# Optimization experiments

Measured on AMD Instinct MI355X. Metric: run time of the kernel, lower is better.

## Reference

```python
import jax, jax.numpy as jnp
import numpy as np


def setup_inputs() -> dict:
    key = jax.random.key(0)
    k1, k2, k3, k4 = jax.random.split(key, 4)
    B, Q, K, H, D = 2, 2048, 2048, 16, 128
    qs = jax.random.normal(k1, (B, Q, H, D), dtype=jnp.float32)
    ks = jax.random.normal(k2, (B, K, H, D), dtype=jnp.float32)
    vs = jax.random.normal(k3, (B, K, H, D), dtype=jnp.float32)
    valid_lens = jax.random.randint(k4, (B,), 1, K + 1, dtype=jnp.int32)
    return {"qs": qs, "ks": ks, "vs": vs, "valid_lens": valid_lens}


def reference(qs, ks, vs, valid_lens):
    B, Q, H, D = qs.shape
    K = ks.shape[1]
    # rearrange 'B L H D -> (B H) L D'
    q = qs.transpose(0, 2, 1, 3).reshape(B * H, Q, D)
    k = ks.transpose(0, 2, 1, 3).reshape(B * H, K, D)
    v = vs.transpose(0, 2, 1, 3).reshape(B * H, K, D)
    # DotScorer: scaled dot product -> (B*H, Q, K)
    scores = jnp.einsum('bqd,bkd->bqk', q, k) / jnp.sqrt(jnp.float32(D))
    # mask_attn: key positions >= valid_len get large negative score
    vl = jnp.repeat(valid_lens, H)                         # (B*H,)
    mask = jnp.arange(K)[None, None, :] < vl[:, None, None]
    scores = jnp.where(mask, scores, jnp.float32(-1e6))
    attn = jax.nn.softmax(scores, axis=-1)
    # dropout is identity (p_dropout=0 / not training)
    ctx = attn @ v                                         # (B*H, Q, D)
    ctx = ctx.reshape(B, H, Q, D).transpose(0, 2, 1, 3)    # (B, Q, H, D)
    return ctx, attn.reshape(B, H, Q, K)
```

## Files before the change

### kernel.cpp

```cpp
#include <hip/hip_runtime.h>
#include <hip/hip_bf16.h>
#include <stdint.h>

#define B_ 2
#define Qn 2048
#define Kn 2048
#define Hn 16
#define Dn 128
#define QT 128
#define KT 64
#define KT1 128
#define HD (Hn*Dn)
#define KROW 132
#define VROW 72

typedef __bf16 bf16x8 __attribute__((ext_vector_type(8)));
typedef __bf16 bf16x4 __attribute__((ext_vector_type(4)));
typedef float f32x4 __attribute__((ext_vector_type(4)));
typedef float f32x16 __attribute__((ext_vector_type(16)));

union BF8 { __bf16 e[8]; bf16x8 v; };

#define SCALE 0.088388347648318447f

struct SMp2 { unsigned short K[2][KT][KROW]; unsigned short V[2][Dn][VROW]; };
union SMu { SMp2 p2; unsigned short K1[2][KT1][KROW]; };

__device__ __forceinline__ void bar_lgkm() {
  asm volatile("s_waitcnt lgkmcnt(0)" ::: "memory");
  __builtin_amdgcn_s_barrier();
  __builtin_amdgcn_sched_barrier(0);
}

__device__ __forceinline__ bf16x4 cvt4(f32x4 a) {
  bf16x4 r;
  r[0] = (__bf16)a[0]; r[1] = (__bf16)a[1];
  r[2] = (__bf16)a[2]; r[3] = (__bf16)a[3];
  return r;
}

__device__ __forceinline__ void stage_k64(const float* kb, unsigned short (*dst)[KROW], int tid) {
  #pragma unroll
  for (int ii = 0; ii < 8; ++ii) {
    int chunk = ii * 256 + tid;
    int row = chunk >> 5, cv = chunk & 31;
    f32x4 a = *(const f32x4*)(kb + (size_t)row * HD + cv * 4);
    *(bf16x4*)&dst[row][cv * 4] = cvt4(a);
  }
}

__device__ __forceinline__ void stage_k128(const float* kb, unsigned short (*dst)[KROW], int tid) {
  #pragma unroll
  for (int ii = 0; ii < 16; ++ii) {
    int chunk = ii * 256 + tid;
    int row = chunk >> 5, cv = chunk & 31;
    f32x4 a = *(const f32x4*)(kb + (size_t)row * HD + cv * 4);
    *(bf16x4*)&dst[row][cv * 4] = cvt4(a);
  }
}

__device__ __forceinline__ void stage_v64(const float* vb, unsigned short (*dst)[VROW], int tid) {
  int d = tid & 127, t0 = tid >> 7;
  const float* colp = vb + d;
  #pragma unroll
  for (int rr = 0; rr < 4; ++rr) {
    int idx = rr * 2 + t0;
    int base = (idx >> 2) * 32 + ((idx >> 1) & 1) * 16 + (idx & 1) * 4;
    BF8 t;
    #pragma unroll
    for (int j = 0; j < 4; ++j) {
      t.e[j]     = (__bf16)colp[(size_t)(base + j) * HD];
      t.e[4 + j] = (__bf16)colp[(size_t)(base + 8 + j) * HD];
    }
    *(bf16x8*)&dst[d][idx * 8] = t.v;
  }
}

__global__ __launch_bounds__(256, 2) void attn_fwd(
    const float* __restrict__ qs, const float* __restrict__ ks,
    const float* __restrict__ vs, const int* __restrict__ vlen,
    float* __restrict__ ctx_out, float* __restrict__ attn_out)
{
  __shared__ __align__(16) SMu sm;

  const int tid = threadIdx.x, wave = tid >> 6, lane = tid & 63;
  const int l31 = lane & 31, hi = lane >> 5;

  const int L   = blockIdx.x;
  const int xcd = L & 7;
  const int i5  = L >> 3;
  const int bh  = ((i5 & 3) << 3) + xcd;
  const int qt  = i5 >> 2;
  const int b   = bh >> 4, h = bh & 15;
  const int vl  = vlen[b];
  const int qbw = qt * QT + wave * 32;

  BF8 qf[8];
  {
    const float* qrow = qs + (((size_t)(b * Qn + qbw + l31)) * Hn + h) * Dn;
    #pragma unroll
    for (int s = 0; s < 8; ++s) {
      int d0 = s * 16 + hi * 8;
      f32x4 a0 = *(const f32x4*)(qrow + d0);
      f32x4 a1 = *(const f32x4*)(qrow + d0 + 4);
      #pragma unroll
      for (int j = 0; j < 4; ++j) { qf[s].e[j] = (__bf16)a0[j]; qf[s].e[4 + j] = (__bf16)a1[j]; }
    }
  }

  const float* kbase = ks + ((size_t)b * Kn * Hn + h) * Dn;
  const float* vbase = vs + ((size_t)b * Kn * Hn + h) * Dn;

  f32x4 rsv = {0.f, 0.f, 0.f, 0.f};
  {
    const int nkt1 = (vl + KT1 - 1) / KT1;
    const bool hasb1 = (vl & (KT1 - 1)) != 0;
    stage_k128(kbase, sm.K1[0], tid);
    bar_lgkm();
    for (int t = 0; t < nkt1; ++t) {
      const int cur = t & 1;
      if (t + 1 < nkt1) stage_k128(kbase + (size_t)(t + 1) * KT1 * HD, sm.K1[cur ^ 1], tid);
      const bool mb = hasb1 && (t == nkt1 - 1);
      #pragma unroll
      for (int m = 0; m < 4; ++m) {
        f32x16 acc;
        #pragma unroll
        for (int i = 0; i < 16; ++i) acc[i] = 0.f;
        #pragma unroll
        for (int s = 0; s < 8; ++s) {
          BF8 kf; kf.v = *(const bf16x8*)&sm.K1[cur][m * 32 + l31][s * 16 + hi * 8];
          acc = __builtin_amdgcn_mfma_f32_32x32x16_bf16(kf.v, qf[s].v, acc, 0, 0, 0);
        }
        if (!mb) {
          #pragma unroll
          for (int reg = 0; reg < 16; ++reg) rsv[reg & 3] += __expf(acc[reg] * SCALE);
        } else {
          const int kb0 = t * KT1 + m * 32 + hi * 4;
          #pragma unroll
          for (int reg = 0; reg < 16; ++reg) {
            int key = kb0 + (reg & 3) + 8 * (reg >> 2);
            rsv[reg & 3] += (key < vl) ? __expf(acc[reg] * SCALE) : 0.f;
          }
        }
      }
      bar_lgkm();
    }
  }
  float rs = (rsv[0] + rsv[1]) + (rsv[2] + rsv[3]);
  rs += __shfl_xor(rs, 32);
  const float inv = 1.0f / rs;

  f32x16 ctxa[4];
  #pragma unroll
  for (int ch = 0; ch < 4; ++ch)
    #pragma unroll
    for (int i = 0; i < 16; ++i) ctxa[ch][i] = 0.f;

  const int nkt = (vl + KT - 1) / KT;
  const bool hasb2 = (vl & (KT - 1)) != 0;
  stage_k64(kbase, sm.p2.K[0], tid);
  stage_v64(vbase, sm.p2.V[0], tid);
  bar_lgkm();
  float* rowp = attn_out + ((size_t)bh * Qn + qbw + l31) * Kn;
  for (int t = 0; t < nkt; ++t) {
    const int cur = t & 1;
    if (t + 1 < nkt) {
      stage_k64(kbase + (size_t)(t + 1) * KT * HD, sm.p2.K[cur ^ 1], tid);
      stage_v64(vbase + (size_t)(t + 1) * KT * HD, sm.p2.V[cur ^ 1], tid);
    }
    const bool mb = hasb2 && (t == nkt - 1);
    #pragma unroll
    for (int m = 0; m < 2; ++m) {
      f32x16 acc;
      #pragma unroll
      for (int i = 0; i < 16; ++i) acc[i] = 0.f;
      #pragma unroll
      for (int s = 0; s < 8; ++s) {
        BF8 kf; kf.v = *(const bf16x8*)&sm.p2.K[cur][m * 32 + l31][s * 16 + hi * 8];
        acc = __builtin_amdgcn_mfma_f32_32x32x16_bf16(kf.v, qf[s].v, acc, 0, 0, 0);
      }
      const int kb0 = t * KT + m * 32;
      BF8 pf0, pf1;
      #pragma unroll
      for (int r4 = 0; r4 < 4; ++r4) {
        f32x4 p;
        if (!mb) {
          #pragma unroll
          for (int rr = 0; rr < 4; ++rr) p[rr] = __expf(acc[r4 * 4 + rr] * SCALE) * inv;
        } else {
          #pragma unroll
          for (int rr = 0; rr < 4; ++rr) {
            int key = kb0 + r4 * 8 + hi * 4 + rr;
            p[rr] = (key < vl) ? __expf(acc[r4 * 4 + rr] * SCALE) * inv : 0.f;
          }
        }
        #pragma unroll
        for (int rr = 0; rr < 4; ++rr) {
          if (r4 < 2) pf0.e[r4 * 4 + rr] = (__bf16)p[rr];
          else        pf1.e[(r4 - 2) * 4 + rr] = (__bf16)p[rr];
        }
        *(f32x4*)(rowp + kb0 + r4 * 8 + hi * 4) = p;
      }
      #pragma unroll
      for (int ch = 0; ch < 4; ++ch) {
        BF8 v0; v0.v = *(const bf16x8*)&sm.p2.V[cur][ch * 32 + l31][(m * 4 + hi) * 8];
        ctxa[ch] = __builtin_amdgcn_mfma_f32_32x32x16_bf16(v0.v, pf0.v, ctxa[ch], 0, 0, 0);
        BF8 v1; v1.v = *(const bf16x8*)&sm.p2.V[cur][ch * 32 + l31][(m * 4 + 2 + hi) * 8];
        ctxa[ch] = __builtin_amdgcn_mfma_f32_32x32x16_bf16(v1.v, pf1.v, ctxa[ch], 0, 0, 0);
      }
    }
    bar_lgkm();
  }

  const int col0 = nkt * KT;
  #pragma unroll 1
  for (int r = 0; r < 32; ++r) {
    float* zp = attn_out + ((size_t)bh * Qn + qbw + r) * Kn;
    for (int c4 = col0 + lane * 4; c4 < Kn; c4 += 256)
      *(f32x4*)(zp + c4) = (f32x4){0.f, 0.f, 0.f, 0.f};
  }

  float* cp = ctx_out + (((size_t)(b * Qn + qbw + l31)) * Hn + h) * Dn;
  #pragma unroll
  for (int ch = 0; ch < 4; ++ch)
    #pragma unroll
    for (int r4 = 0; r4 < 4; ++r4) {
      f32x4 o;
      #pragma unroll
      for (int rr = 0; rr < 4; ++rr) o[rr] = ctxa[ch][r4 * 4 + rr];
      *(f32x4*)(cp + ch * 32 + r4 * 8 + hi * 4) = o;
    }
}

extern "C" void kernel_launch(void* const* d_in, const int* in_sizes, int n_in,
                              void* d_out, int out_size, void* d_ws, size_t ws_size,
                              hipStream_t stream) {
  const float* qs   = (const float*)d_in[0];
  const float* ks   = (const float*)d_in[1];
  const float* vs   = (const float*)d_in[2];
  const int*   vlen = (const int*)d_in[3];
  float* ctx  = (float*)d_out;
  float* attn = ctx + (size_t)B_ * Qn * Hn * Dn;
  attn_fwd<<<dim3((Qn / QT) * B_ * Hn), 256, 0, stream>>>(qs, ks, vs, vlen, ctx, attn);
}
```

Before: 228.8 us.

## Pre-convert K/V to swizzled bf16 images and stream tiles via global_load_lds

```diff
diff --git a/kernel.cpp b/kernel.cpp
--- a/kernel.cpp
+++ b/kernel.cpp
@@ -11,26 +11,24 @@
 #define KT 64
 #define KT1 128
 #define HD (Hn*Dn)
-#define KROW 132
-#define VROW 72
 
 typedef __bf16 bf16x8 __attribute__((ext_vector_type(8)));
 typedef __bf16 bf16x4 __attribute__((ext_vector_type(4)));
 typedef float f32x4 __attribute__((ext_vector_type(4)));
 typedef float f32x16 __attribute__((ext_vector_type(16)));
+typedef unsigned short u16x8 __attribute__((ext_vector_type(8)));
 
 union BF8 { __bf16 e[8]; bf16x8 v; };
+union U16x8 { unsigned short u[8]; u16x8 v; };
 
 #define SCALE 0.088388347648318447f
-
-struct SMp2 { unsigned short K[2][KT][KROW]; unsigned short V[2][Dn][VROW]; };
-union SMu { SMp2 p2; unsigned short K1[2][KT1][KROW]; };
-
-__device__ __forceinline__ void bar_lgkm() {
-  asm volatile("s_waitcnt lgkmcnt(0)" ::: "memory");
-  __builtin_amdgcn_s_barrier();
-  __builtin_amdgcn_sched_barrier(0);
-}
+#define SCL2  (0.088388347648318447f * 1.4426950408889634f)
+
+#if __has_builtin(__builtin_amdgcn_exp2f)
+#define EXP2(x) __builtin_amdgcn_exp2f(x)
+#else
+#define EXP2(x) exp2f(x)
+#endif
 
 __device__ __forceinline__ bf16x4 cvt4(f32x4 a) {
   bf16x4 r;
@@ -39,49 +37,85 @@
   return r;
 }
 
-__device__ __forceinline__ void stage_k64(const float* kb, unsigned short (*dst)[KROW], int tid) {
-  #pragma unroll
-  for (int ii = 0; ii < 8; ++ii) {
-    int chunk = ii * 256 + tid;
-    int row = chunk >> 5, cv = chunk & 31;
-    f32x4 a = *(const f32x4*)(kb + (size_t)row * HD + cv * 4);
-    *(bf16x4*)&dst[row][cv * 4] = cvt4(a);
-  }
-}
-
-__device__ __forceinline__ void stage_k128(const float* kb, unsigned short (*dst)[KROW], int tid) {
-  #pragma unroll
-  for (int ii = 0; ii < 16; ++ii) {
-    int chunk = ii * 256 + tid;
-    int row = chunk >> 5, cv = chunk & 31;
-    f32x4 a = *(const f32x4*)(kb + (size_t)row * HD + cv * 4);
-    *(bf16x4*)&dst[row][cv * 4] = cvt4(a);
-  }
-}
-
-__device__ __forceinline__ void stage_v64(const float* vb, unsigned short (*dst)[VROW], int tid) {
-  int d = tid & 127, t0 = tid >> 7;
-  const float* colp = vb + d;
-  #pragma unroll
-  for (int rr = 0; rr < 4; ++rr) {
-    int idx = rr * 2 + t0;
-    int base = (idx >> 2) * 32 + ((idx >> 1) & 1) * 16 + (idx & 1) * 4;
-    BF8 t;
+__global__ __launch_bounds__(256) void conv_k(const float* __restrict__ ks,
+                                              unsigned short* __restrict__ kws) {
+  const int blk = blockIdx.x;
+  const int bh = blk >> 4, t = blk & 15;
+  const int b = bh >> 4, h = bh & 15;
+  const int tid = threadIdx.x;
+  const float* src = ks + ((size_t)(b * Kn + t * 128) * Hn + h) * Dn;
+  unsigned short* dst = kws + (size_t)blk * 16384;
+  #pragma unroll
+  for (int i = 0; i < 8; ++i) {
+    int idx = i * 256 + tid;
+    int row = idx >> 4, sp = idx & 15;
+    int slot = (sp - row) & 15;
+    const float* s2 = src + (size_t)row * HD + slot * 8;
+    f32x4 a0 = *(const f32x4*)s2;
+    f32x4 a1 = *(const f32x4*)(s2 + 4);
+    U16x8 o;
+    *(bf16x4*)&o.u[0] = cvt4(a0);
+    *(bf16x4*)&o.u[4] = cvt4(a1);
+    *(u16x8*)(dst + (size_t)idx * 8) = o.v;
+  }
+}
+
+__global__ __launch_bounds__(256) void conv_v(const float* __restrict__ vs,
+                                              unsigned short* __restrict__ vws) {
+  __shared__ unsigned short l[64 * 132];
+  const int blk = blockIdx.x;
+  const int bh = blk >> 5, t = blk & 31;
+  const int b = bh >> 4, h = bh & 15;
+  const int tid = threadIdx.x;
+  const float* src = vs + ((size_t)(b * Kn + t * 64) * Hn + h) * Dn;
+  #pragma unroll
+  for (int i = 0; i < 8; ++i) {
+    int idx = i * 256 + tid;
+    int k = idx >> 5, dc = idx & 31;
+    f32x4 a = *(const f32x4*)(src + (size_t)k * HD + dc * 4);
+    *(bf16x4*)&l[k * 132 + dc * 4] = cvt4(a);
+  }
+  __syncthreads();
+  unsigned short* dst = vws + (size_t)blk * 8192;
+  #pragma unroll
+  for (int i = 0; i < 4; ++i) {
+    int idx = i * 256 + tid;
+    int d = idx >> 3, ds = idx & 7;
+    int c = (ds - d) & 7;
+    int kb = ((c >> 2) * 32) + (((c >> 1) & 1) * 16) + ((c & 1) * 4);
+    U16x8 o;
     #pragma unroll
     for (int j = 0; j < 4; ++j) {
-      t.e[j]     = (__bf16)colp[(size_t)(base + j) * HD];
-      t.e[4 + j] = (__bf16)colp[(size_t)(base + 8 + j) * HD];
-    }
-    *(bf16x8*)&dst[d][idx * 8] = t.v;
-  }
-}
+      o.u[j]     = l[(kb + j) * 132 + d];
+      o.u[4 + j] = l[(kb + 8 + j) * 132 + d];
+    }
+    *(u16x8*)(dst + (size_t)idx * 8) = o.v;
+  }
+}
+
+__device__ __forceinline__ void dma16(const void* g, void* l) {
+  __builtin_amdgcn_global_load_lds((const __attribute__((address_space(1))) void*)g,
+                                   (__attribute__((address_space(3))) void*)l, 16, 0, 0);
+}
+__device__ __forceinline__ void dma_tile(const char* gsrc, char* lds, int tid, int n4k) {
+  const int off  = tid * 16;
+  const int woff = (tid & 192) * 16;
+  #pragma unroll
+  for (int i = 0; i < n4k; ++i)
+    dma16(gsrc + i * 4096 + off, lds + i * 4096 + woff);
+}
+
+#define WAITBAR do { \
+  asm volatile("s_waitcnt vmcnt(0) lgkmcnt(0)" ::: "memory"); \
+  __builtin_amdgcn_s_barrier(); \
+  __builtin_amdgcn_sched_barrier(0); } while (0)
 
 __global__ __launch_bounds__(256, 2) void attn_fwd(
-    const float* __restrict__ qs, const float* __restrict__ ks,
-    const float* __restrict__ vs, const int* __restrict__ vlen,
+    const float* __restrict__ qs, const int* __restrict__ vlen,
+    const char* __restrict__ kimg, const char* __restrict__ vimg,
     float* __restrict__ ctx_out, float* __restrict__ attn_out)
 {
-  __shared__ __align__(16) SMu sm;
+  __shared__ __align__(16) char smraw[65536];
 
   const int tid = threadIdx.x, wave = tid >> 6, lane = tid & 63;
   const int l31 = lane & 31, hi = lane >> 5;
@@ -95,6 +129,14 @@
   const int vl  = vlen[b];
   const int qbw = qt * QT + wave * 32;
 
+  int vaddrK[8], vaddrV[4];
+  #pragma unroll
+  for (int s = 0; s < 8; ++s)
+    vaddrK[s] = l31 * 256 + (((2 * s + hi + l31) & 15) << 4);
+  #pragma unroll
+  for (int j = 0; j < 4; ++j)
+    vaddrV[j] = l31 * 128 + ((((hi + 2 * j) + l31) & 7) << 4);
+
   BF8 qf[8];
   {
     const float* qrow = qs + (((size_t)(b * Qn + qbw + l31)) * Hn + h) * Dn;
@@ -104,23 +146,27 @@
       f32x4 a0 = *(const f32x4*)(qrow + d0);
       f32x4 a1 = *(const f32x4*)(qrow + d0 + 4);
       #pragma unroll
-      for (int j = 0; j < 4; ++j) { qf[s].e[j] = (__bf16)a0[j]; qf[s].e[4 + j] = (__bf16)a1[j]; }
-    }
-  }
-
-  const float* kbase = ks + ((size_t)b * Kn * Hn + h) * Dn;
-  const float* vbase = vs + ((size_t)b * Kn * Hn + h) * Dn;
+      for (int j = 0; j < 4; ++j) {
+        qf[s].e[j]     = (__bf16)(a0[j] * SCL2);
+        qf[s].e[4 + j] = (__bf16)(a1[j] * SCL2);
+      }
+    }
+  }
+
+  const char* kimg_bh = kimg + ((size_t)(bh * 16) << 15);
+  const char* vimg_bh = vimg + ((size_t)(bh * 32) << 14);
 
   f32x4 rsv = {0.f, 0.f, 0.f, 0.f};
   {
     const int nkt1 = (vl + KT1 - 1) / KT1;
     const bool hasb1 = (vl & (KT1 - 1)) != 0;
-    stage_k128(kbase, sm.K1[0], tid);
-    bar_lgkm();
+    dma_tile(kimg_bh, smraw, tid, 8);
+    WAITBAR;
     for (int t = 0; t < nkt1; ++t) {
       const int cur = t & 1;
-      if (t + 1 < nkt1) stage_k128(kbase + (size_t)(t + 1) * KT1 * HD, sm.K1[cur ^ 1], tid);
+      if (t + 1 < nkt1) dma_tile(kimg_bh + ((size_t)(t + 1) << 15), smraw + ((cur ^ 1) << 15), tid, 8);
       const bool mb = hasb1 && (t == nkt1 - 1);
+      const char* kb_l = smraw + (cur << 15);
       #pragma unroll
       for (int m = 0; m < 4; ++m) {
         f32x16 acc;
@@ -128,22 +174,22 @@
         for (int i = 0; i < 16; ++i) acc[i] = 0.f;
         #pragma unroll
         for (int s = 0; s < 8; ++s) {
-          BF8 kf; kf.v = *(const bf16x8*)&sm.K1[cur][m * 32 + l31][s * 16 + hi * 8];
+          BF8 kf; kf.v = *(const bf16x8*)(kb_l + m * 8192 + vaddrK[s]);
           acc = __builtin_amdgcn_mfma_f32_32x32x16_bf16(kf.v, qf[s].v, acc, 0, 0, 0);
         }
         if (!mb) {
           #pragma unroll
-          for (int reg = 0; reg < 16; ++reg) rsv[reg & 3] += __expf(acc[reg] * SCALE);
+          for (int reg = 0; reg < 16; ++reg) rsv[reg & 3] += EXP2(acc[reg]);
         } else {
           const int kb0 = t * KT1 + m * 32 + hi * 4;
           #pragma unroll
           for (int reg = 0; reg < 16; ++reg) {
             int key = kb0 + (reg & 3) + 8 * (reg >> 2);
-            rsv[reg & 3] += (key < vl) ? __expf(acc[reg] * SCALE) : 0.f;
+            rsv[reg & 3] += (key < vl) ? EXP2(acc[reg]) : 0.f;
           }
         }
       }
-      bar_lgkm();
+      WAITBAR;
     }
   }
   float rs = (rsv[0] + rsv[1]) + (rsv[2] + rsv[3]);
@@ -158,17 +204,21 @@
 
   const int nkt = (vl + KT - 1) / KT;
   const bool hasb2 = (vl & (KT - 1)) != 0;
-  stage_k64(kbase, sm.p2.K[0], tid);
-  stage_v64(vbase, sm.p2.V[0], tid);
-  bar_lgkm();
+  dma_tile(kimg_bh, smraw, tid, 4);
+  dma_tile(vimg_bh, smraw + 32768, tid, 4);
+  WAITBAR;
   float* rowp = attn_out + ((size_t)bh * Qn + qbw + l31) * Kn;
   for (int t = 0; t < nkt; ++t) {
     const int cur = t & 1;
     if (t + 1 < nkt) {
-      stage_k64(kbase + (size_t)(t + 1) * KT * HD, sm.p2.K[cur ^ 1], tid);
-      stage_v64(vbase + (size_t)(t + 1) * KT * HD, sm.p2.V[cur ^ 1], tid);
+      const int tn = t + 1;
+      dma_tile(kimg_bh + ((size_t)(tn >> 1) << 15) + ((size_t)(tn & 1) << 14),
+               smraw + ((cur ^ 1) << 14), tid, 4);
+      dma_tile(vimg_bh + ((size_t)tn << 14), smraw + 32768 + ((cur ^ 1) << 14), tid, 4);
     }
     const bool mb = hasb2 && (t == nkt - 1);
+    const char* kb_l = smraw + (cur << 14);
+    const char* vb_l = smraw + 32768 + (cur << 14);
     #pragma unroll
     for (int m = 0; m < 2; ++m) {
       f32x16 acc;
@@ -176,7 +226,7 @@
       for (int i = 0; i < 16; ++i) acc[i] = 0.f;
       #pragma unroll
       for (int s = 0; s < 8; ++s) {
-        BF8 kf; kf.v = *(const bf16x8*)&sm.p2.K[cur][m * 32 + l31][s * 16 + hi * 8];
+        BF8 kf; kf.v = *(const bf16x8*)(kb_l + m * 8192 + vaddrK[s]);
         acc = __builtin_amdgcn_mfma_f32_32x32x16_bf16(kf.v, qf[s].v, acc, 0, 0, 0);
       }
       const int kb0 = t * KT + m * 32;
@@ -186,12 +236,12 @@
         f32x4 p;
         if (!mb) {
           #pragma unroll
-          for (int rr = 0; rr < 4; ++rr) p[rr] = __expf(acc[r4 * 4 + rr] * SCALE) * inv;
+          for (int rr = 0; rr < 4; ++rr) p[rr] = EXP2(acc[r4 * 4 + rr]) * inv;
         } else {
           #pragma unroll
           for (int rr = 0; rr < 4; ++rr) {
             int key = kb0 + r4 * 8 + hi * 4 + rr;
-            p[rr] = (key < vl) ? __expf(acc[r4 * 4 + rr] * SCALE) * inv : 0.f;
+            p[rr] = (key < vl) ? EXP2(acc[r4 * 4 + rr]) * inv : 0.f;
           }
         }
         #pragma unroll
@@ -203,13 +253,13 @@
       }
       #pragma unroll
       for (int ch = 0; ch < 4; ++ch) {
-        BF8 v0; v0.v = *(const bf16x8*)&sm.p2.V[cur][ch * 32 + l31][(m * 4 + hi) * 8];
+        BF8 v0; v0.v = *(const bf16x8*)(vb_l + ch * 4096 + vaddrV[2 * m]);
         ctxa[ch] = __builtin_amdgcn_mfma_f32_32x32x16_bf16(v0.v, pf0.v, ctxa[ch], 0, 0, 0);
-        BF8 v1; v1.v = *(const bf16x8*)&sm.p2.V[cur][ch * 32 + l31][(m * 4 + 2 + hi) * 8];
+        BF8 v1; v1.v = *(const bf16x8*)(vb_l + ch * 4096 + vaddrV[2 * m + 1]);
         ctxa[ch] = __builtin_amdgcn_mfma_f32_32x32x16_bf16(v1.v, pf1.v, ctxa[ch], 0, 0, 0);
       }
     }
-    bar_lgkm();
+    WAITBAR;
   }
 
   const int col0 = nkt * KT;
@@ -220,6 +270,197 @@
       *(f32x4*)(zp + c4) = (f32x4){0.f, 0.f, 0.f, 0.f};
   }
 
+  float* cp = ctx_out + (((size_t)(b * Qn + qbw + l31)) * Hn + h) * Dn;
+  #pragma unroll
+  for (int ch = 0; ch < 4; ++ch)
+    #pragma unroll
+    for (int r4 = 0; r4 < 4; ++r4) {
+      f32x4 o;
+      #pragma unroll
+      for (int rr = 0; rr < 4; ++rr) o[rr] = ctxa[ch][r4 * 4 + rr];
+      *(f32x4*)(cp + ch * 32 + r4 * 8 + hi * 4) = o;
+    }
+}
+
+#define KROW 132
+#define VROW 72
+struct SMp2f { unsigned short K[2][KT][KROW]; unsigned short V[2][Dn][VROW]; };
+union SMuf { SMp2f p2; unsigned short K1[2][KT1][KROW]; };
+
+__device__ __forceinline__ void bar_lgkm() {
+  asm volatile("s_waitcnt lgkmcnt(0)" ::: "memory");
+  __builtin_amdgcn_s_barrier();
+  __builtin_amdgcn_sched_barrier(0);
+}
+__device__ __forceinline__ void fb_stage_k64(const float* kb, unsigned short (*dst)[KROW], int tid) {
+  #pragma unroll
+  for (int ii = 0; ii < 8; ++ii) {
+    int chunk = ii * 256 + tid;
+    int row = chunk >> 5, cv = chunk & 31;
+    f32x4 a = *(const f32x4*)(kb + (size_t)row * HD + cv * 4);
+    *(bf16x4*)&dst[row][cv * 4] = cvt4(a);
+  }
+}
+__device__ __forceinline__ void fb_stage_k128(const float* kb, unsigned short (*dst)[KROW], int tid) {
+  #pragma unroll
+  for (int ii = 0; ii < 16; ++ii) {
+    int chunk = ii * 256 + tid;
+    int row = chunk >> 5, cv = chunk & 31;
+    f32x4 a = *(const f32x4*)(kb + (size_t)row * HD + cv * 4);
+    *(bf16x4*)&dst[row][cv * 4] = cvt4(a);
+  }
+}
+__device__ __forceinline__ void fb_stage_v64(const float* vb, unsigned short (*dst)[VROW], int tid) {
+  int d = tid & 127, t0 = tid >> 7;
+  const float* colp = vb + d;
+  #pragma unroll
+  for (int rr = 0; rr < 4; ++rr) {
+    int idx = rr * 2 + t0;
+    int base = (idx >> 2) * 32 + ((idx >> 1) & 1) * 16 + (idx & 1) * 4;
+    BF8 t;
+    #pragma unroll
+    for (int j = 0; j < 4; ++j) {
+      t.e[j]     = (__bf16)colp[(size_t)(base + j) * HD];
+      t.e[4 + j] = (__bf16)colp[(size_t)(base + 8 + j) * HD];
+    }
+    *(bf16x8*)&dst[d][idx * 8] = t.v;
+  }
+}
+__global__ __launch_bounds__(256, 2) void attn_fwd_fb(
+    const float* __restrict__ qs, const float* __restrict__ ks,
+    const float* __restrict__ vs, const int* __restrict__ vlen,
+    float* __restrict__ ctx_out, float* __restrict__ attn_out)
+{
+  __shared__ __align__(16) SMuf sm;
+  const int tid = threadIdx.x, wave = tid >> 6, lane = tid & 63;
+  const int l31 = lane & 31, hi = lane >> 5;
+  const int L = blockIdx.x, xcd = L & 7, i5 = L >> 3;
+  const int bh = ((i5 & 3) << 3) + xcd, qt = i5 >> 2;
+  const int b = bh >> 4, h = bh & 15;
+  const int vl = vlen[b];
+  const int qbw = qt * QT + wave * 32;
+  BF8 qf[8];
+  {
+    const float* qrow = qs + (((size_t)(b * Qn + qbw + l31)) * Hn + h) * Dn;
+    #pragma unroll
+    for (int s = 0; s < 8; ++s) {
+      int d0 = s * 16 + hi * 8;
+      f32x4 a0 = *(const f32x4*)(qrow + d0);
+      f32x4 a1 = *(const f32x4*)(qrow + d0 + 4);
+      #pragma unroll
+      for (int j = 0; j < 4; ++j) {
+        qf[s].e[j] = (__bf16)(a0[j] * SCL2);
+        qf[s].e[4 + j] = (__bf16)(a1[j] * SCL2);
+      }
+    }
+  }
+  const float* kbase = ks + ((size_t)b * Kn * Hn + h) * Dn;
+  const float* vbase = vs + ((size_t)b * Kn * Hn + h) * Dn;
+  f32x4 rsv = {0.f, 0.f, 0.f, 0.f};
+  {
+    const int nkt1 = (vl + KT1 - 1) / KT1;
+    const bool hasb1 = (vl & (KT1 - 1)) != 0;
+    fb_stage_k128(kbase, sm.K1[0], tid);
+    bar_lgkm();
+    for (int t = 0; t < nkt1; ++t) {
+      const int cur = t & 1;
+      if (t + 1 < nkt1) fb_stage_k128(kbase + (size_t)(t + 1) * KT1 * HD, sm.K1[cur ^ 1], tid);
+      const bool mb = hasb1 && (t == nkt1 - 1);
+      #pragma unroll
+      for (int m = 0; m < 4; ++m) {
+        f32x16 acc;
+        #pragma unroll
+        for (int i = 0; i < 16; ++i) acc[i] = 0.f;
+        #pragma unroll
+        for (int s = 0; s < 8; ++s) {
+          BF8 kf; kf.v = *(const bf16x8*)&sm.K1[cur][m * 32 + l31][s * 16 + hi * 8];
+          acc = __builtin_amdgcn_mfma_f32_32x32x16_bf16(kf.v, qf[s].v, acc, 0, 0, 0);
+        }
+        if (!mb) {
+          #pragma unroll
+          for (int reg = 0; reg < 16; ++reg) rsv[reg & 3] += EXP2(acc[reg]);
+        } else {
+          const int kb0 = t * KT1 + m * 32 + hi * 4;
+          #pragma unroll
+          for (int reg = 0; reg < 16; ++reg) {
+            int key = kb0 + (reg & 3) + 8 * (reg >> 2);
+            rsv[reg & 3] += (key < vl) ? EXP2(acc[reg]) : 0.f;
+          }
+        }
+      }
+      bar_lgkm();
+    }
+  }
+  float rs = (rsv[0] + rsv[1]) + (rsv[2] + rsv[3]);
+  rs += __shfl_xor(rs, 32);
+  const float inv = 1.0f / rs;
+  f32x16 ctxa[4];
+  #pragma unroll
+  for (int ch = 0; ch < 4; ++ch)
+    #pragma unroll
+    for (int i = 0; i < 16; ++i) ctxa[ch][i] = 0.f;
+  const int nkt = (vl + KT - 1) / KT;
+  const bool hasb2 = (vl & (KT - 1)) != 0;
+  fb_stage_k64(kbase, sm.p2.K[0], tid);
+  fb_stage_v64(vbase, sm.p2.V[0], tid);
+  bar_lgkm();
+  float* rowp = attn_out + ((size_t)bh * Qn + qbw + l31) * Kn;
+  for (int t = 0; t < nkt; ++t) {
+    const int cur = t & 1;
+    if (t + 1 < nkt) {
+      fb_stage_k64(kbase + (size_t)(t + 1) * KT * HD, sm.p2.K[cur ^ 1], tid);
+      fb_stage_v64(vbase + (size_t)(t + 1) * KT * HD, sm.p2.V[cur ^ 1], tid);
+    }
+    const bool mb = hasb2 && (t == nkt - 1);
+    #pragma unroll
+    for (int m = 0; m < 2; ++m) {
+      f32x16 acc;
+      #pragma unroll
+      for (int i = 0; i < 16; ++i) acc[i] = 0.f;
+      #pragma unroll
+      for (int s = 0; s < 8; ++s) {
+        BF8 kf; kf.v = *(const bf16x8*)&sm.p2.K[cur][m * 32 + l31][s * 16 + hi * 8];
+        acc = __builtin_amdgcn_mfma_f32_32x32x16_bf16(kf.v, qf[s].v, acc, 0, 0, 0);
+      }
+      const int kb0 = t * KT + m * 32;
+      BF8 pf0, pf1;
+      #pragma unroll
+      for (int r4 = 0; r4 < 4; ++r4) {
+        f32x4 p;
+        if (!mb) {
+          #pragma unroll
+          for (int rr = 0; rr < 4; ++rr) p[rr] = EXP2(acc[r4 * 4 + rr]) * inv;
+        } else {
+          #pragma unroll
+          for (int rr = 0; rr < 4; ++rr) {
+            int key = kb0 + r4 * 8 + hi * 4 + rr;
+            p[rr] = (key < vl) ? EXP2(acc[r4 * 4 + rr]) * inv : 0.f;
+          }
+        }
+        #pragma unroll
+        for (int rr = 0; rr < 4; ++rr) {
+          if (r4 < 2) pf0.e[r4 * 4 + rr] = (__bf16)p[rr];
+          else        pf1.e[(r4 - 2) * 4 + rr] = (__bf16)p[rr];
+        }
+        *(f32x4*)(rowp + kb0 + r4 * 8 + hi * 4) = p;
+      }
+      #pragma unroll
+      for (int ch = 0; ch < 4; ++ch) {
+        BF8 v0; v0.v = *(const bf16x8*)&sm.p2.V[cur][ch * 32 + l31][(m * 4 + hi) * 8];
+        ctxa[ch] = __builtin_amdgcn_mfma_f32_32x32x16_bf16(v0.v, pf0.v, ctxa[ch], 0, 0, 0);
+        BF8 v1; v1.v = *(const bf16x8*)&sm.p2.V[cur][ch * 32 + l31][(m * 4 + 2 + hi) * 8];
+        ctxa[ch] = __builtin_amdgcn_mfma_f32_32x32x16_bf16(v1.v, pf1.v, ctxa[ch], 0, 0, 0);
+      }
+    }
+    bar_lgkm();
+  }
+  const int col0 = nkt * KT;
+  #pragma unroll 1
+  for (int r = 0; r < 32; ++r) {
+    float* zp = attn_out + ((size_t)bh * Qn + qbw + r) * Kn;
+    for (int c4 = col0 + lane * 4; c4 < Kn; c4 += 256)
+      *(f32x4*)(zp + c4) = (f32x4){0.f, 0.f, 0.f, 0.f};
+  }
   float* cp = ctx_out + (((size_t)(b * Qn + qbw + l31)) * Hn + h) * Dn;
   #pragma unroll
   for (int ch = 0; ch < 4; ++ch)
@@ -241,5 +482,15 @@
   const int*   vlen = (const int*)d_in[3];
   float* ctx  = (float*)d_out;
   float* attn = ctx + (size_t)B_ * Qn * Hn * Dn;
-  attn_fwd<<<dim3((Qn / QT) * B_ * Hn), 256, 0, stream>>>(qs, ks, vs, vlen, ctx, attn);
-}
+
+  if (ws_size >= ((size_t)32 << 20)) {
+    unsigned short* kws = (unsigned short*)d_ws;
+    unsigned short* vws = kws + ((size_t)8 << 20);
+    conv_k<<<dim3(512), 256, 0, stream>>>(ks, kws);
+    conv_v<<<dim3(1024), 256, 0, stream>>>(vs, vws);
+    attn_fwd<<<dim3((Qn / QT) * B_ * Hn), 256, 0, stream>>>(
+        qs, vlen, (const char*)kws, (const char*)vws, ctx, attn);
+  } else {
+    attn_fwd_fb<<<dim3((Qn / QT) * B_ * Hn), 256, 0, stream>>>(qs, ks, vs, vlen, ctx, attn);
+  }
+}
```

Result: faster. 205.6 us (-10.2%).
